# Optimization experiments

Measured on AMD Instinct MI355X. Metric: run time of the kernel, lower is better.

The kernel has to match this reference:

```python
import jax, jax.numpy as jnp
import numpy as np

# lct_fk config (matches init_kwargs)
BIN_LEN = 0.01
WALL_SIZE = 2.0
C_LIGHT = 3.0e8


def _safe_sqrt(v):
    # sqrt(relu(v)) with a well-defined (zero) subgradient at v<=0
    pos = v > 0
    return jnp.where(pos, jnp.sqrt(jnp.where(pos, v, 1.0)), 0.0)


def _trilinear_zero(vol, pz, py, px):
    # vol: (D,H,W) complex64; pz/py/px: (D2,H2,W2) float pixel coords
    # Trilinear sampling with zeros padding (== F.grid_sample align_corners=False)
    D, H, W = vol.shape
    z0f = jnp.floor(pz); y0f = jnp.floor(py); x0f = jnp.floor(px)
    dz = pz - z0f; dy = py - y0f; dx = px - x0f
    z0 = z0f.astype(jnp.int32); y0 = y0f.astype(jnp.int32); x0 = x0f.astype(jnp.int32)
    out = jnp.zeros(pz.shape, vol.dtype)
    for iz, wz in ((z0, 1.0 - dz), (z0 + 1, dz)):
        for iy, wy in ((y0, 1.0 - dy), (y0 + 1, dy)):
            for ix, wx in ((x0, 1.0 - dx), (x0 + 1, dx)):
                valid = (iz >= 0) & (iz < D) & (iy >= 0) & (iy < H) & (ix >= 0) & (ix < W)
                v = vol[jnp.clip(iz, 0, D - 1), jnp.clip(iy, 0, H - 1), jnp.clip(ix, 0, W - 1)]
                w = jnp.where(valid, wz * wy * wx, 0.0)
                out = out + w * v
    return out


def setup_inputs() -> dict:
    key = jax.random.key(0)
    feture = jax.random.uniform(key, (1, 2, 128, 128, 128), dtype=jnp.float32)
    return {"feture_bxdxtxhxw": feture}


def reference(feture_bxdxtxhxw):
    b, d, T, H, W = feture_bxdxtxhxw.shape
    M, N = T, H  # temprol_grid (== crop), sptial_grid; tbes=0, tens=crop -> no temporal pad
    width = WALL_SIZE / 2.0
    trange = M * BIN_LEN  # crop * c * (bin_len/c)

    # z-weighting: (z/(M-1))^2, then sqrt(relu(.))
    gridz = (jnp.arange(M, dtype=jnp.float32) / (M - 1)).reshape(1, M, 1, 1)
    data = feture_bxdxtxhxw.reshape(b * d, T, H, W) * (gridz ** 2)
    data = _safe_sqrt(jax.nn.relu(data))

    # zero-pad to (2T,2H,2W), FFT, fftshift (roll by half == fftshift for even sizes)
    datapad = jnp.pad(data, ((0, 0), (0, M), (0, N), (0, N)))
    fre = jnp.fft.fftshift(jnp.fft.fftn(datapad, axes=(-3, -2, -1)), axes=(-3, -2, -1))

    # Stolt (f-k) warped coordinates, normalized to [-1,1]
    zdim = (jnp.arange(2 * M, dtype=jnp.float32) - M) / M
    xdim = (jnp.arange(2 * N, dtype=jnp.float32) - N) / N
    gz = zdim[:, None, None]            # varies along axis 0
    gy = xdim[None, :, None]            # varies along axis 1
    gx = xdim[None, None, :]            # varies along axis 2
    fk = (N * trange / (M * width * 4.0)) ** 2
    gznew = jnp.sqrt(fk * (gx ** 2 + gy ** 2) + gz ** 2)  # (2M,2N,2N)
    gznew = jnp.broadcast_to(gznew, (2 * M, 2 * N, 2 * N))

    # unnormalize (align_corners=False): pix = ((c+1)*size - 1)/2
    px = ((jnp.broadcast_to(gx, gznew.shape) + 1.0) * (2 * N) - 1.0) * 0.5
    py = ((jnp.broadcast_to(gy, gznew.shape) + 1.0) * (2 * N) - 1.0) * 0.5
    pz = ((gznew + 1.0) * (2 * M) - 1.0) * 0.5

    samp = jax.vmap(lambda v: _trilinear_zero(v, pz, py, px))(fre)

    # zero negative/zero frequencies along z, then Stolt Jacobian scaling
    z0pos = M + 1  # first index where zdim > 0
    zmask = (jnp.arange(2 * M) >= z0pos)[None, :, None, None]
    samp = samp * zmask
    samp = samp * (jnp.abs(gz) / (gznew + 1e-8))[None]

    samp = jnp.fft.fftshift(samp, axes=(-3, -2, -1))  # ifftshift == fftshift (even dims)
    vol = jnp.fft.ifftn(samp, axes=(-3, -2, -1))
    out = vol[:, :M, :N, :N].real
    return out.reshape(b, d, M, N, N)
```

## Files before the change

### kernel.cpp

```cpp
#include <hip/hip_runtime.h>

static constexpr size_t VS   = 8388608;
static constexpr int    ZSTR = 65536;
static constexpr int    YSTR = 256;
static constexpr size_t VSB  = 4194304;
static constexpr int    BZS  = 32768;
static constexpr int    BYS  = 128;
static constexpr int    LSTR = 261;

typedef float vf2 __attribute__((ext_vector_type(2)));

__device__ __forceinline__ vf2 cmul(vf2 a, vf2 b){
    vf2 asw; asw.x = -a.y; asw.y = a.x;
    return a*b.x + asw*b.y;
}

constexpr int BREV(int k){ return ((k&1)<<3)|((k&2)<<1)|((k&4)>>1)|((k&8)>>3); }

__device__ __forceinline__ void bf(vf2& a, vf2& b, float c, float s){
    vf2 sum = a + b;
    vf2 dif = a - b;
    vf2 dsw; dsw.x = -dif.y; dsw.y = dif.x;
    b = dif*c + dsw*s;
    a = sum;
}

template<int DIR>
__device__ __forceinline__ void fft16(vf2 r[16]){
    constexpr float D = (float)DIR;
    constexpr float C16[8] = {1.f, 0.92387953f, 0.70710678f, 0.38268343f, 0.f, -0.38268343f, -0.70710678f, -0.92387953f};
    constexpr float S16[8] = {0.f, 0.38268343f, 0.70710678f, 0.92387953f, 1.f, 0.92387953f, 0.70710678f, 0.38268343f};
#pragma unroll
    for (int j = 0; j < 8; ++j) bf(r[j], r[j+8], C16[j], D*S16[j]);
    constexpr float C8[4] = {1.f, 0.70710678f, 0.f, -0.70710678f};
    constexpr float S8[4] = {0.f, 0.70710678f, 1.f, 0.70710678f};
#pragma unroll
    for (int g = 0; g < 16; g += 8)
#pragma unroll
        for (int j = 0; j < 4; ++j) bf(r[g+j], r[g+j+4], C8[j], D*S8[j]);
#pragma unroll
    for (int g = 0; g < 16; g += 4){
        bf(r[g],   r[g+2], 1.f, 0.f);
        bf(r[g+1], r[g+3], 0.f, D);
    }
#pragma unroll
    for (int g = 0; g < 16; g += 2) bf(r[g], r[g+1], 1.f, 0.f);
}

__device__ __forceinline__ void init_tw(vf2* tw, float dir){
    int tid = threadIdx.x;
    float ang = dir * 0.0245436926f * (float)((tid >> 4)*(tid & 15));
    float s, c; __sincosf(ang, &s, &c);
    vf2 w; w.x = c; w.y = s;
    tw[tid] = w;
}

template<int DIR>
__device__ __forceinline__ void mid256s(vf2 r[16], vf2* sh8, const vf2* tw, int t, int l){
    fft16<DIR>(r);
#pragma unroll
    for (int k1 = 1; k1 < 16; ++k1)
        r[BREV(k1)] = cmul(r[BREV(k1)], tw[k1*16 + t]);
    int lr = l & 7;
    bool lo = (l < 8);
    __syncthreads();
    if (lo){
#pragma unroll
        for (int k1 = 0; k1 < 16; ++k1) sh8[lr*LSTR + k1*16 + (t ^ k1)] = r[BREV(k1)];
    }
    __syncthreads();
    if (lo){
#pragma unroll
        for (int n2 = 0; n2 < 16; ++n2) r[n2] = sh8[lr*LSTR + t*16 + (n2 ^ t)];
    }
    __syncthreads();
    if (!lo){
#pragma unroll
        for (int k1 = 0; k1 < 16; ++k1) sh8[lr*LSTR + k1*16 + (t ^ k1)] = r[BREV(k1)];
    }
    __syncthreads();
    if (!lo){
#pragma unroll
        for (int n2 = 0; n2 < 16; ++n2) r[n2] = sh8[lr*LSTR + t*16 + (n2 ^ t)];
    }
    fft16<DIR>(r);
}

template<int DIR, int NIN, int NOUT>
__device__ __forceinline__ void fft_strided(vf2* g, int S){
    __shared__ vf2 sh8[8*LSTR];
    __shared__ vf2 tw[256];
    int t = threadIdx.x >> 4, l = threadIdx.x & 15;
    vf2 r[16];
    vf2 zero; zero.x = 0.f; zero.y = 0.f;
#pragma unroll
    for (int n1 = 0; n1 < 16; ++n1)
        r[n1] = (n1 < NIN/16) ? g[(size_t)(16*n1 + t)*S + l] : zero;
    init_tw(tw, (float)DIR);
    __syncthreads();
    mid256s<DIR>(r, sh8, tw, t, l);
#pragma unroll
    for (int k2 = 0; k2 < 16; ++k2)
        if (k2 < NOUT/16) g[(size_t)(t + 16*k2)*S + l] = r[BREV(k2)];
}

__global__ void __launch_bounds__(256) k_p1(const float* __restrict__ in, vf2* __restrict__ A){
    __shared__ vf2 sh8[8*LSTR];
    __shared__ vf2 tw[256];
    __shared__ float shin[16*130];
    init_tw(tw, -1.f);
    int th = threadIdx.x, bid = blockIdx.x;
    int yc = bid & 7, z = (bid >> 3) & 127, v = bid >> 10;
    float gz = z * (1.0f/127.0f);
    float g2 = gz*gz;
    const float* src = in + (((size_t)(v*128 + z))*128 + yc*16)*128;
    for (int idx = th; idx < 2048; idx += 256){
        float val = src[idx] * g2;
        shin[(idx >> 7)*130 + (idx & 127)] = val > 0.f ? sqrtf(val) : 0.f;
    }
    __syncthreads();
    int t = th >> 4, l = th & 15;
    vf2 r[16];
    vf2 zero; zero.x = 0.f; zero.y = 0.f;
#pragma unroll
    for (int n1 = 0; n1 < 16; ++n1){
        r[n1] = zero;
        if (n1 < 8) r[n1].x = shin[l*130 + 16*n1 + t];
    }
    mid256s<-1>(r, sh8, tw, t, l);
    int lr = l & 7;
    vf2* dst = A + (size_t)v*VS + (size_t)z*ZSTR + (size_t)(yc*16)*YSTR;
#pragma unroll
    for (int half = 0; half < 2; ++half){
        __syncthreads();
        if ((l >> 3) == half){
#pragma unroll
            for (int k2 = 0; k2 < 16; ++k2) sh8[lr*LSTR + t + 16*k2] = r[BREV(k2)];
        }
        __syncthreads();
        vf2* d2 = dst + half*8*YSTR;
        for (int idx = th; idx < 2048; idx += 256){
            int line = idx >> 8, k = idx & 255;
            vf2 a = sh8[line*LSTR + k];
            vf2 p = sh8[line*LSTR + ((k - 1) & 255)];
            if (k == 128) p = zero;
            d2[idx] = (a + p)*0.5f;
        }
    }
}

__global__ void __launch_bounds__(256) k_p2z(vf2* __restrict__ A){
    int bid = blockIdx.x;
    int xb = bid & 15, y = (bid >> 4) & 127, v = bid >> 11;
    fft_strided<-1,128,128>(A + (size_t)v*VS + (size_t)y*YSTR + xb*16, ZSTR);
}

__global__ void __launch_bounds__(256) k_p3y(vf2* __restrict__ A){
    __shared__ vf2 sh8[8*LSTR];
    __shared__ vf2 tw[256];
    int bid = blockIdx.x;
    int xb = bid & 15, z = (bid >> 4) & 127, v = bid >> 11;
    vf2* g = A + (size_t)v*VS + (size_t)z*ZSTR + xb*16;
    int t = threadIdx.x >> 4, l = threadIdx.x & 15;
    vf2 r[16];
    vf2 zero; zero.x = 0.f; zero.y = 0.f;
#pragma unroll
    for (int n1 = 0; n1 < 16; ++n1)
        r[n1] = (n1 < 8) ? g[(size_t)(16*n1 + t)*YSTR + l] : zero;
    init_tw(tw, -1.f);
    __syncthreads();
    mid256s<-1>(r, sh8, tw, t, l);
    int lr = l & 7;
#pragma unroll
    for (int half = 0; half < 2; ++half){
        __syncthreads();
        if ((l >> 3) == half){
#pragma unroll
            for (int k2 = 0; k2 < 16; ++k2) sh8[lr*LSTR + t + 16*k2] = r[BREV(k2)];
        }
        __syncthreads();
        if ((l >> 3) == half){
#pragma unroll
            for (int k2 = 0; k2 < 16; ++k2){
                int k = t + 16*k2;
                vf2 a = sh8[lr*LSTR + k];
                vf2 p = sh8[lr*LSTR + ((k - 1) & 255)];
                if (k == 128) p = zero;
                g[(size_t)k*YSTR + l] = (a + p)*0.5f;
            }
        }
    }
}

__global__ void __launch_bounds__(256) k_p45(const vf2* __restrict__ A, vf2* __restrict__ B){
    __shared__ vf2 sh8[8*LSTR];
    __shared__ vf2 tw[256];
    init_tw(tw, 1.f);
    int tid = threadIdx.x, bid = blockIdx.x;
    int yc = bid & 15, zn = (bid >> 4) & 127, v = bid >> 11;
    const vf2* Av = A + (size_t)v*VS;
    int t = tid & 15, l = tid >> 4;
    int yn = yc*16 + l;
    float gy = (yn < 128 ? yn : yn - 256) * (1.0f/128.0f);
    float gz = zn * (1.0f/128.0f);
    float c2 = 0.1024f*gy*gy + gz*gz;
    unsigned rowoff = (unsigned)yn*YSTR;
    vf2 r[16];
#pragma unroll
    for (int n1 = 0; n1 < 16; ++n1){
        int xn = 16*n1 + t;
        float gx = (xn < 128 ? xn : xn - 256) * (1.0f/128.0f);
        float s2 = c2 + 0.1024f*gx*gx;
        float rs = __builtin_amdgcn_rsqf(s2 + 1e-12f);
        float gznew = s2 * rs;
        float pz = gznew*128.0f + 127.5f;
        int zi = (int)pz;
        float dz = pz - (float)zi;
        int zp0 = zi - 128;
        float wf = gz * rs;
        float w0 = (((unsigned)zp0     < 128u) ? (1.0f - dz) : 0.f) * wf;
        float w1 = (((unsigned)(zp0+1) < 128u) ? dz : 0.f) * wf;
        vf2 v0 = Av[(size_t)((unsigned)(zp0 & 127) * ZSTR) + rowoff + xn];
        vf2 v1 = Av[(size_t)((unsigned)((zp0 + 1) & 127) * ZSTR) + rowoff + xn];
        r[n1] = v0*w0 + v1*w1;
    }
    __syncthreads();
    mid256s<1>(r, sh8, tw, t, l);
    vf2* dst = B + (size_t)v*VSB + (size_t)zn*BZS + (size_t)yn*BYS;
#pragma unroll
    for (int k2 = 0; k2 < 8; ++k2)
        dst[t + 16*k2] = r[BREV(k2)];
}

__global__ void __launch_bounds__(256) k_p6(vf2* __restrict__ B){
    int bid = blockIdx.x;
    int xb = bid & 7, zn = (bid >> 3) & 127, v = bid >> 10;
    fft_strided<1,256,128>(B + (size_t)v*VSB + (size_t)zn*BZS + xb*16, BYS);
}

__global__ void __launch_bounds__(256) k_p7(const vf2* __restrict__ B, float* __restrict__ out){
    __shared__ vf2 sh8[8*LSTR];
    __shared__ vf2 tw[256];
    int bid = blockIdx.x;
    int xb = bid & 7, y = (bid >> 3) & 127, v = bid >> 10;
    const vf2* g = B + (size_t)v*VSB + (size_t)y*BYS + xb*16;
    int t = threadIdx.x >> 4, l = threadIdx.x & 15;
    vf2 r[16];
    vf2 zero; zero.x = 0.f; zero.y = 0.f;
#pragma unroll
    for (int n1 = 0; n1 < 16; ++n1)
        r[n1] = (n1 < 8) ? g[(size_t)(16*n1 + t)*BZS + l] : zero;
    init_tw(tw, 1.f);
    __syncthreads();
    mid256s<1>(r, sh8, tw, t, l);
    const float sc = 1.0f/16777216.0f;
    float* dst = out + ((size_t)(v*128)*128 + y)*128 + xb*16 + l;
#pragma unroll
    for (int k2 = 0; k2 < 8; ++k2)
        dst[(size_t)(t + 16*k2)*16384] = r[BREV(k2)].x * sc;
}

extern "C" void kernel_launch(void* const* d_in, const int* in_sizes, int n_in,
                              void* d_out, int out_size, void* d_ws, size_t ws_size,
                              hipStream_t stream){
    const float* in = (const float*)d_in[0];
    float* out = (float*)d_out;
    vf2* A = (vf2*)d_ws;
    vf2* B = A + 2*VS;
    k_p1 <<< 2048, 256, 0, stream>>>(in, A);
    k_p2z<<< 4096, 256, 0, stream>>>(A);
    k_p3y<<< 4096, 256, 0, stream>>>(A);
    k_p45<<< 4096, 256, 0, stream>>>(A, B);
    k_p6 <<< 2048, 256, 0, stream>>>(B);
    k_p7 <<< 2048, 256, 0, stream>>>(B, out);
}
```

Baseline: 203.3 us.

## Widen strided FFT blocks to 32 columns with 512 threads

```diff
diff --git a/kernel.cpp b/kernel.cpp
--- a/kernel.cpp
+++ b/kernel.cpp
@@ -49,10 +49,12 @@
 
 __device__ __forceinline__ void init_tw(vf2* tw, float dir){
     int tid = threadIdx.x;
-    float ang = dir * 0.0245436926f * (float)((tid >> 4)*(tid & 15));
-    float s, c; __sincosf(ang, &s, &c);
-    vf2 w; w.x = c; w.y = s;
-    tw[tid] = w;
+    if (tid < 256){
+        float ang = dir * 0.0245436926f * (float)((tid >> 4)*(tid & 15));
+        float s, c; __sincosf(ang, &s, &c);
+        vf2 w; w.x = c; w.y = s;
+        tw[tid] = w;
+    }
 }
 
 template<int DIR>
@@ -86,11 +88,42 @@
     fft16<DIR>(r);
 }
 
+template<int DIR>
+__device__ __forceinline__ void mid256w(vf2 r[16], vf2* sh16, const vf2* tw, int t, int l){
+    fft16<DIR>(r);
+#pragma unroll
+    for (int k1 = 1; k1 < 16; ++k1)
+        r[BREV(k1)] = cmul(r[BREV(k1)], tw[k1*16 + t]);
+    int lr = l & 15;
+    bool lo = (l < 16);
+    __syncthreads();
+    if (lo){
+#pragma unroll
+        for (int k1 = 0; k1 < 16; ++k1) sh16[lr*LSTR + k1*16 + (t ^ k1)] = r[BREV(k1)];
+    }
+    __syncthreads();
+    if (lo){
+#pragma unroll
+        for (int n2 = 0; n2 < 16; ++n2) r[n2] = sh16[lr*LSTR + t*16 + (n2 ^ t)];
+    }
+    __syncthreads();
+    if (!lo){
+#pragma unroll
+        for (int k1 = 0; k1 < 16; ++k1) sh16[lr*LSTR + k1*16 + (t ^ k1)] = r[BREV(k1)];
+    }
+    __syncthreads();
+    if (!lo){
+#pragma unroll
+        for (int n2 = 0; n2 < 16; ++n2) r[n2] = sh16[lr*LSTR + t*16 + (n2 ^ t)];
+    }
+    fft16<DIR>(r);
+}
+
 template<int DIR, int NIN, int NOUT>
-__device__ __forceinline__ void fft_strided(vf2* g, int S){
-    __shared__ vf2 sh8[8*LSTR];
-    __shared__ vf2 tw[256];
-    int t = threadIdx.x >> 4, l = threadIdx.x & 15;
+__device__ __forceinline__ void fft_stridedw(vf2* g, int S){
+    __shared__ vf2 sh16[16*LSTR];
+    __shared__ vf2 tw[256];
+    int t = threadIdx.x >> 5, l = threadIdx.x & 31;
     vf2 r[16];
     vf2 zero; zero.x = 0.f; zero.y = 0.f;
 #pragma unroll
@@ -98,7 +131,7 @@
         r[n1] = (n1 < NIN/16) ? g[(size_t)(16*n1 + t)*S + l] : zero;
     init_tw(tw, (float)DIR);
     __syncthreads();
-    mid256s<DIR>(r, sh8, tw, t, l);
+    mid256w<DIR>(r, sh16, tw, t, l);
 #pragma unroll
     for (int k2 = 0; k2 < 16; ++k2)
         if (k2 < NOUT/16) g[(size_t)(t + 16*k2)*S + l] = r[BREV(k2)];
@@ -149,19 +182,19 @@
     }
 }
 
-__global__ void __launch_bounds__(256) k_p2z(vf2* __restrict__ A){
+__global__ void __launch_bounds__(512) k_p2z(vf2* __restrict__ A){
     int bid = blockIdx.x;
-    int xb = bid & 15, y = (bid >> 4) & 127, v = bid >> 11;
-    fft_strided<-1,128,128>(A + (size_t)v*VS + (size_t)y*YSTR + xb*16, ZSTR);
-}
-
-__global__ void __launch_bounds__(256) k_p3y(vf2* __restrict__ A){
-    __shared__ vf2 sh8[8*LSTR];
+    int xb = bid & 7, y = (bid >> 3) & 127, v = bid >> 10;
+    fft_stridedw<-1,128,128>(A + (size_t)v*VS + (size_t)y*YSTR + xb*32, ZSTR);
+}
+
+__global__ void __launch_bounds__(512) k_p3y(vf2* __restrict__ A){
+    __shared__ vf2 sh16[16*LSTR];
     __shared__ vf2 tw[256];
     int bid = blockIdx.x;
-    int xb = bid & 15, z = (bid >> 4) & 127, v = bid >> 11;
-    vf2* g = A + (size_t)v*VS + (size_t)z*ZSTR + xb*16;
-    int t = threadIdx.x >> 4, l = threadIdx.x & 15;
+    int xb = bid & 7, z = (bid >> 3) & 127, v = bid >> 10;
+    vf2* g = A + (size_t)v*VS + (size_t)z*ZSTR + xb*32;
+    int t = threadIdx.x >> 5, l = threadIdx.x & 31;
     vf2 r[16];
     vf2 zero; zero.x = 0.f; zero.y = 0.f;
 #pragma unroll
@@ -169,25 +202,22 @@
         r[n1] = (n1 < 8) ? g[(size_t)(16*n1 + t)*YSTR + l] : zero;
     init_tw(tw, -1.f);
     __syncthreads();
-    mid256s<-1>(r, sh8, tw, t, l);
-    int lr = l & 7;
+    mid256w<-1>(r, sh16, tw, t, l);
+    int lr = l & 15;
 #pragma unroll
     for (int half = 0; half < 2; ++half){
         __syncthreads();
-        if ((l >> 3) == half){
-#pragma unroll
-            for (int k2 = 0; k2 < 16; ++k2) sh8[lr*LSTR + t + 16*k2] = r[BREV(k2)];
+        if ((l >> 4) == half){
+#pragma unroll
+            for (int k2 = 0; k2 < 16; ++k2) sh16[lr*LSTR + t + 16*k2] = r[BREV(k2)];
         }
         __syncthreads();
-        if ((l >> 3) == half){
-#pragma unroll
-            for (int k2 = 0; k2 < 16; ++k2){
-                int k = t + 16*k2;
-                vf2 a = sh8[lr*LSTR + k];
-                vf2 p = sh8[lr*LSTR + ((k - 1) & 255)];
-                if (k == 128) p = zero;
-                g[(size_t)k*YSTR + l] = (a + p)*0.5f;
-            }
+        for (int idx = threadIdx.x; idx < 4096; idx += 512){
+            int k = idx >> 4, col = idx & 15;
+            vf2 a = sh16[col*LSTR + k];
+            vf2 p = sh16[col*LSTR + ((k - 1) & 255)];
+            if (k == 128) p = zero;
+            g[(size_t)k*YSTR + half*16 + col] = (a + p)*0.5f;
         }
     }
 }
@@ -232,19 +262,19 @@
         dst[t + 16*k2] = r[BREV(k2)];
 }
 
-__global__ void __launch_bounds__(256) k_p6(vf2* __restrict__ B){
+__global__ void __launch_bounds__(512) k_p6(vf2* __restrict__ B){
     int bid = blockIdx.x;
-    int xb = bid & 7, zn = (bid >> 3) & 127, v = bid >> 10;
-    fft_strided<1,256,128>(B + (size_t)v*VSB + (size_t)zn*BZS + xb*16, BYS);
-}
-
-__global__ void __launch_bounds__(256) k_p7(const vf2* __restrict__ B, float* __restrict__ out){
-    __shared__ vf2 sh8[8*LSTR];
+    int xb = bid & 3, zn = (bid >> 2) & 127, v = bid >> 9;
+    fft_stridedw<1,256,128>(B + (size_t)v*VSB + (size_t)zn*BZS + xb*32, BYS);
+}
+
+__global__ void __launch_bounds__(512) k_p7(const vf2* __restrict__ B, float* __restrict__ out){
+    __shared__ vf2 sh16[16*LSTR];
     __shared__ vf2 tw[256];
     int bid = blockIdx.x;
-    int xb = bid & 7, y = (bid >> 3) & 127, v = bid >> 10;
-    const vf2* g = B + (size_t)v*VSB + (size_t)y*BYS + xb*16;
-    int t = threadIdx.x >> 4, l = threadIdx.x & 15;
+    int xb = bid & 3, y = (bid >> 2) & 127, v = bid >> 9;
+    const vf2* g = B + (size_t)v*VSB + (size_t)y*BYS + xb*32;
+    int t = threadIdx.x >> 5, l = threadIdx.x & 31;
     vf2 r[16];
     vf2 zero; zero.x = 0.f; zero.y = 0.f;
 #pragma unroll
@@ -252,9 +282,9 @@
         r[n1] = (n1 < 8) ? g[(size_t)(16*n1 + t)*BZS + l] : zero;
     init_tw(tw, 1.f);
     __syncthreads();
-    mid256s<1>(r, sh8, tw, t, l);
+    mid256w<1>(r, sh16, tw, t, l);
     const float sc = 1.0f/16777216.0f;
-    float* dst = out + ((size_t)(v*128)*128 + y)*128 + xb*16 + l;
+    float* dst = out + ((size_t)(v*128)*128 + y)*128 + xb*32 + l;
 #pragma unroll
     for (int k2 = 0; k2 < 8; ++k2)
         dst[(size_t)(t + 16*k2)*16384] = r[BREV(k2)].x * sc;
@@ -268,9 +298,9 @@
     vf2* A = (vf2*)d_ws;
     vf2* B = A + 2*VS;
     k_p1 <<< 2048, 256, 0, stream>>>(in, A);
-    k_p2z<<< 4096, 256, 0, stream>>>(A);
-    k_p3y<<< 4096, 256, 0, stream>>>(A);
+    k_p2z<<< 2048, 512, 0, stream>>>(A);
+    k_p3y<<< 2048, 512, 0, stream>>>(A);
     k_p45<<< 4096, 256, 0, stream>>>(A, B);
-    k_p6 <<< 2048, 256, 0, stream>>>(B);
-    k_p7 <<< 2048, 256, 0, stream>>>(B, out);
-}
+    k_p6 <<< 1024, 512, 0, stream>>>(B);
+    k_p7 <<< 1024, 512, 0, stream>>>(B, out);
+}
```

After: 203.6 us. No clear change (+0.1%).
